# Kernel tuning notes

Hardware: AMD Instinct MI355X
Metric: run time of the kernel (lower is better)

Reference implementation:

```python
import jax, jax.numpy as jnp
import numpy as np

ROPE_BASE = 10000.0


def _rope(x):
    # x: (B, S, H, D) -- rotate-half RoPE applied per head over the sequence dim
    B, S, H, D = x.shape
    half = D // 2
    inv_freq = 1.0 / (ROPE_BASE ** (jnp.arange(half, dtype=jnp.float32) / half))
    ang = jnp.arange(S, dtype=jnp.float32)[:, None] * inv_freq[None, :]  # (S, half)
    cos = jnp.cos(ang)[None, :, None, :].astype(x.dtype)
    sin = jnp.sin(ang)[None, :, None, :].astype(x.dtype)
    x1, x2 = x[..., :half], x[..., half:]
    return jnp.concatenate([x1 * cos - x2 * sin, x2 * cos + x1 * sin], axis=-1)


def setup_inputs() -> dict:
    key = jax.random.key(0)
    ks = jax.random.split(key, 7)
    B, S, D = 8, 1024, 512
    HD = 512  # num_heads * key_dim = 8 * 64
    scale = 0.02
    return {
        "query": jax.random.normal(ks[0], (B, S, D), dtype=jnp.float32),
        "value": jax.random.normal(ks[1], (B, S, D), dtype=jnp.float32),
        "key_in": jax.random.normal(ks[2], (B, S, D), dtype=jnp.float32),
        "Wq": jax.random.normal(ks[3], (D, HD), dtype=jnp.float32) * scale,
        "Wk": jax.random.normal(ks[4], (D, HD), dtype=jnp.float32) * scale,
        "Wv": jax.random.normal(ks[5], (D, HD), dtype=jnp.float32) * scale,
        "Wo": jax.random.normal(ks[6], (HD, D), dtype=jnp.float32) * scale,
    }


def reference(query, value, key_in, Wq, Wk, Wv, Wo):
    H, Dh = 8, 64
    B, Sq, _ = query.shape
    Sk = key_in.shape[1]
    # QKV projections, split heads: (B, S, H, Dh)
    q = (query @ Wq).reshape(B, Sq, H, Dh)
    v = (value @ Wv).reshape(B, Sk, H, Dh)
    k = (key_in @ Wk).reshape(B, Sk, H, Dh)
    # inline RoPE on q and k (applied before head transpose, as in the original)
    q = _rope(q)
    k = _rope(k)
    # scaled dot-product attention with causal mask
    q = q * (1.0 / jnp.sqrt(jnp.asarray(Dh, q.dtype)))
    scores = jnp.einsum("bqhd,bkhd->bhqk", q, k)  # (B, H, Sq, Sk)
    causal = jnp.tril(jnp.ones((Sq, Sk), dtype=bool))[None, None]
    scores = jnp.where(causal, scores, jnp.asarray(-1e9, scores.dtype))
    probs = jax.nn.softmax(scores, axis=-1)
    out = jnp.einsum("bhqk,bkhd->bqhd", probs, v)  # (B, Sq, H, Dh)
    out = out.reshape(B, Sq, H * Dh) @ Wo  # output projection
    return out
```

## Files before the change

### kernel.cpp

```cpp
#include <hip/hip_runtime.h>
#include <hip/hip_bf16.h>
#include <stdint.h>

#define DEV static __device__ __forceinline__

typedef __attribute__((ext_vector_type(8)))  short    s16x8;
typedef __attribute__((ext_vector_type(4)))  short    s16x4;
typedef __attribute__((ext_vector_type(8)))  __bf16   bf16x8;
typedef __attribute__((ext_vector_type(2)))  __bf16   bf16x2;
typedef __attribute__((ext_vector_type(4)))  float    f32x4;
typedef __attribute__((ext_vector_type(16))) float    f32x16;
typedef __attribute__((ext_vector_type(2)))  unsigned u32x2;
typedef __attribute__((ext_vector_type(4)))  unsigned u32x4;

#define WAIT_VMCNT(N) do{ asm volatile("s_waitcnt vmcnt(" #N ")" ::: "memory"); \
                          __builtin_amdgcn_sched_barrier(0); }while(0)
DEV void barrier_raw(){ __builtin_amdgcn_sched_barrier(0); __builtin_amdgcn_s_barrier(); }

DEV short f2b(float f){
  union{float f; uint32_t i;} x; x.f = f;
  uint32_t r = x.i + 0x7FFFu + ((x.i >> 16) & 1u);
  return (short)(r >> 16);
}
DEV unsigned packbf(float a, float b){
  bf16x2 v = { (__bf16)a, (__bf16)b };
  return __builtin_bit_cast(unsigned, v);
}
DEV bf16x8 as_bf(s16x8 v){ return __builtin_bit_cast(bf16x8, v); }
DEV float fexp2(float x){ return __builtin_amdgcn_exp2f(x); }
DEV f32x4 mf(s16x8 a, s16x8 b, f32x4 c){
  return __builtin_amdgcn_mfma_f32_16x16x32_bf16(as_bf(a), as_bf(b), c, 0, 0, 0);
}
DEV f32x16 mf32(s16x8 a, s16x8 b, f32x16 c){
  return __builtin_amdgcn_mfma_f32_32x32x16_bf16(as_bf(a), as_bf(b), c, 0, 0, 0);
}

DEV void gload_lds16(const void* g, void* l){
  __builtin_amdgcn_global_load_lds((const __attribute__((address_space(1))) void*)g,
                                   (__attribute__((address_space(3))) void*)l, 16, 0, 0);
}

#if __has_builtin(__builtin_amdgcn_permlane32_swap)
DEV void pswap2(unsigned a, unsigned b, unsigned& x, unsigned& y){
  u32x2 rr = __builtin_amdgcn_permlane32_swap(a, b, false, false);
  x = rr[0]; y = rr[1];
}
DEV float partner32(float v, int hi){
  unsigned u = __builtin_bit_cast(unsigned, v);
  u32x2 rr = __builtin_amdgcn_permlane32_swap(u, u, false, false);
  return __builtin_bit_cast(float, hi ? rr[0] : rr[1]);
}
#else
DEV void pswap2(unsigned a, unsigned b, unsigned& x, unsigned& y){
  unsigned pa_ = (unsigned)__shfl_xor((int)a, 32, 64);
  unsigned pb_ = (unsigned)__shfl_xor((int)b, 32, 64);
  int lo = ((threadIdx.x & 63) < 32);
  x = lo ? a   : pb_;
  y = lo ? pa_ : b;
}
DEV float partner32(float v, int hi){ (void)hi; return __shfl_xor(v, 32, 64); }
#endif

__global__ __launch_bounds__(256) void k_conv3(const float* __restrict__ q,
                                               const float* __restrict__ k,
                                               const float* __restrict__ v,
                                               short* __restrict__ out){
  int z = blockIdx.z;
  const float* in = (z == 0) ? q : (z == 1) ? k : v;
  int i = (blockIdx.x * 256 + threadIdx.x) * 4;
  float4 val = *(const float4*)(in + i);
  short o[4] = { f2b(val.x), f2b(val.y), f2b(val.z), f2b(val.w) };
  *(uint2*)(out + (size_t)z * 4194304 + i) = *(uint2*)o;
}

__global__ __launch_bounds__(256) void k_wt4(const float* __restrict__ w0,
                                             const float* __restrict__ w1,
                                             const float* __restrict__ w2,
                                             const float* __restrict__ w3,
                                             short* __restrict__ wt){
  __shared__ float tile[32][33];
  int z = blockIdx.z;
  const float* w = (z == 0) ? w0 : (z == 1) ? w1 : (z == 2) ? w2 : w3;
  short* o = wt + (size_t)z * 262144;
  int bx = blockIdx.x * 32, by = blockIdx.y * 32;
  int tx = threadIdx.x, ty = threadIdx.y;
  for (int j = 0; j < 32; j += 8)
    tile[ty + j][tx] = w[(size_t)(by + ty + j) * 512 + bx + tx];
  __syncthreads();
  for (int j = 0; j < 32; j += 8)
    o[(size_t)(bx + ty + j) * 512 + by + tx] = f2b(tile[tx][ty + j]);
}

__global__ __launch_bounds__(256) void k_table(float* __restrict__ tab){
  int idx = blockIdx.x * 256 + threadIdx.x;
  int s = idx >> 5, j = idx & 31;
  float inv = __expf(-(float)j * (1.0f / 32.0f) * logf(10000.0f));
  float ang = (float)s * inv;
  tab[idx * 2 + 0] = cosf(ang);
  tab[idx * 2 + 1] = sinf(ang);
}

__global__ __launch_bounds__(256) void k_qkv(const short* __restrict__ Xb,
                                             const short* __restrict__ Wcat,
                                             const float* __restrict__ tab,
                                             short* __restrict__ Qa,
                                             short* __restrict__ Ka,
                                             short* __restrict__ Vt){
  __shared__ __align__(16) short Al[3][4096];
  __shared__ __align__(16) short Bl[3][4096];
  const int t = threadIdx.x, w = t >> 6, lane = t & 63, fr = lane & 15, fg = lane >> 4;
  const int sel = blockIdx.y >> 2;
  const short* X = Xb + (size_t)sel * 4194304;
  const int bm = blockIdx.x * 128, bn = blockIdx.y * 128;
  const int wm = (w >> 1) * 64, wn = (w & 1) * 64;

  auto stage = [&](int buf, int k0){
#pragma unroll
    for (int q = 0; q < 2; q++){
      int lin = q * 256 + t;
      int row = lin >> 2, sl = lin & 3;
      int gs = (sl ^ (row & 3)) * 8;
      gload_lds16(X    + (size_t)(bm + row) * 512 + k0 + gs, &Al[buf][(q * 256 + w * 64) * 8]);
      gload_lds16(Wcat + (size_t)(bn + row) * 512 + k0 + gs, &Bl[buf][(q * 256 + w * 64) * 8]);
    }
  };

  f32x4 acc[4][4] = {};
  stage(0, 0);
  stage(1, 32);
  for (int t16 = 0; t16 < 16; ++t16){
    barrier_raw();
    int kc = t16 + 2; if (kc > 15) kc = 15;
    stage((t16 + 2) % 3, kc * 32);
    WAIT_VMCNT(8);
    barrier_raw();
    const int cur = t16 % 3;
    s16x8 af[4], bv[4];
#pragma unroll
    for (int f = 0; f < 4; f++){
      int ra = wm + f * 16 + fr;
      af[f] = *(const s16x8*)(&Al[cur][ra * 32 + ((fg ^ (ra & 3)) * 8)]);
      int rb = wn + f * 16 + fr;
      bv[f] = *(const s16x8*)(&Bl[cur][rb * 32 + ((fg ^ (rb & 3)) * 8)]);
    }
#pragma unroll
    for (int i = 0; i < 4; i++)
#pragma unroll
      for (int jj = 0; jj < 4; jj++)
        acc[i][jj] = mf(af[i], bv[jj], acc[i][jj]);
  }

  const int row0 = bm + wm + fg * 4;
  const int b = row0 >> 10;
  const int s_base = row0 & 1023;
  const int hh = (((blockIdx.y & 3) * 128) + wn) >> 6;
  if (sel < 2){
    const float scale = (sel == 0) ? 0.125f * 1.44269504f : 1.0f;
    short* out = (sel == 0) ? Qa : Ka;
#pragma unroll
    for (int i = 0; i < 4; i++)
#pragma unroll
      for (int jj = 0; jj < 2; jj++){
        int d = jj * 16 + fr;
#pragma unroll
        for (int r = 0; r < 4; r++){
          int s = s_base + i * 16 + r;
          float2 cs = *(const float2*)(tab + (size_t)(s * 32 + d) * 2);
          float x1 = acc[i][jj][r], x2 = acc[i][jj + 2][r];
          size_t ob = ((size_t)((b * 8 + hh) * 1024 + s)) * 64 + d;
          out[ob]      = f2b((x1 * cs.x - x2 * cs.y) * scale);
          out[ob + 32] = f2b((x2 * cs.x + x1 * cs.y) * scale);
        }
      }
  } else {
#pragma unroll
    for (int i = 0; i < 4; i++)
#pragma unroll
      for (int jj = 0; jj < 4; jj++){
        int d = jj * 16 + fr;
        s16x4 pk;
#pragma unroll
        for (int r = 0; r < 4; r++) pk[r] = f2b(acc[i][jj][r]);
        size_t ob = ((size_t)((b * 8 + hh) * 64 + d)) * 1024 + s_base + i * 16;
        *(s16x4*)(Vt + ob) = pk;
      }
  }
}

__global__ __launch_bounds__(256) void k_attn(const short* __restrict__ Qb,
                                              const short* __restrict__ Kb,
                                              const short* __restrict__ Vt,
                                              short* __restrict__ O){
  __shared__ __align__(16) short KL[3][4096];
  __shared__ __align__(16) short VL[3][4096];
  const int bid = blockIdx.x;
  const int BiMap[8] = {7,6,5,4, 0,1,2,3};
  const int Bi = BiMap[bid >> 6];
  const int bh = bid & 63;
  const int B0 = Bi * 128;
  const int nch = (B0 >> 6) + 2;
  const int t = threadIdx.x, w = t >> 6, lane = t & 63;
  const int col = lane & 31, hi = lane >> 5;
  const short* Qp = Qb + (size_t)bh * 65536;
  const short* Kp = Kb + (size_t)bh * 65536;
  const short* Vp = Vt + (size_t)bh * 65536;
  const int qrow = B0 + 4 * col + w;

  s16x8 qb[4];
#pragma unroll
  for (int ks = 0; ks < 4; ks++)
    qb[ks] = *(const s16x8*)(Qp + (size_t)qrow * 64 + ks * 16 + hi * 8);

  int crow[16];
#pragma unroll
  for (int r = 0; r < 16; r++) crow[r] = (r & 3) + 8 * (r >> 2) + 4 * hi;

  f32x16 oacc[2] = {};
  float m = -1e30f, l = 0.f;

  auto stage = [&](int buf, int kv0){
#pragma unroll
    for (int R = 0; R < 2; R++){
      int lin = R * 256 + w * 64 + lane;
      int row = lin >> 3, slot = lin & 7;
      int gs = ((slot ^ (row & 7)) * 8);
      gload_lds16(Kp + (size_t)(kv0 + row) * 64 + gs, &KL[buf][(R * 256 + w * 64) * 8]);
      gload_lds16(Vp + (size_t)row * 1024 + kv0 + gs, &VL[buf][(R * 256 + w * 64) * 8]);
    }
  };

  stage(0, 0);
  stage(1, (nch > 1 ? 64 : 0));

  for (int i = 0; i < nch; ++i){
    const int kv0 = i * 64;
    barrier_raw();
    int kc = i + 2; if (kc > nch - 1) kc = nch - 1;
    stage((i + 2) % 3, kc * 64);
    WAIT_VMCNT(8);
    barrier_raw();
    const int cur = i % 3;
    __builtin_amdgcn_s_setprio(1);
    f32x16 sc[2];
#pragma unroll
    for (int f = 0; f < 2; f++){
      f32x16 s = {};
      int row = f * 32 + col, rx = row & 7;
#pragma unroll
      for (int ks = 0; ks < 4; ks++){
        s16x8 ka = *(const s16x8*)(&KL[cur][row * 64 + ((ks * 2 + hi) ^ rx) * 8]);
        s = mf32(ka, qb[ks], s);
      }
      sc[f] = s;
    }
    __builtin_amdgcn_s_setprio(0);
    if (kv0 >= B0){
#pragma unroll
      for (int f = 0; f < 2; f++)
#pragma unroll
        for (int r = 0; r < 16; r++){
          int kv = kv0 + f * 32 + crow[r];
          if (kv > qrow) sc[f][r] = -1e30f;
        }
    }
    float mx[16];
#pragma unroll
    for (int r = 0; r < 16; r++) mx[r] = fmaxf(sc[0][r], sc[1][r]);
#pragma unroll
    for (int off = 8; off >= 1; off >>= 1)
#pragma unroll
      for (int r = 0; r < off; r++) mx[r] = fmaxf(mx[r], mx[r + off]);
    float tm = fmaxf(mx[0], partner32(mx[0], hi));
    if (!__all(tm <= m + 8.f)){
      float mn = fmaxf(m, tm);
      float corr = fexp2(m - mn);
      m = mn;
      l *= corr;
      float cpv[16];
#pragma unroll
      for (int r = 0; r < 16; r++) cpv[r] = __shfl(corr, crow[r], 64);
#pragma unroll
      for (int r = 0; r < 16; r++){ oacc[0][r] *= cpv[r]; oacc[1][r] *= cpv[r]; }
    }
    float p[32];
#pragma unroll
    for (int f = 0; f < 2; f++)
#pragma unroll
      for (int i2 = 0; i2 < 16; i2++) p[f * 16 + i2] = fexp2(sc[f][i2] - m);
    unsigned wq[2][8];
#pragma unroll
    for (int f = 0; f < 2; f++)
#pragma unroll
      for (int i2 = 0; i2 < 8; i2++)
        wq[f][i2] = packbf(p[f * 16 + 2 * i2], p[f * 16 + 2 * i2 + 1]);
#pragma unroll
    for (int off = 16; off >= 1; off >>= 1)
#pragma unroll
      for (int r = 0; r < off; r++) p[r] += p[r + off];
    l += p[0] + partner32(p[0], hi);
    s16x8 pa[4];
#pragma unroll
    for (int f = 0; f < 2; f++)
#pragma unroll
      for (int half = 0; half < 2; half++){
        unsigned w0, w1, w2, w3;
        pswap2(wq[f][half * 4 + 0], wq[f][half * 4 + 2], w0, w2);
        pswap2(wq[f][half * 4 + 1], wq[f][half * 4 + 3], w1, w3);
        u32x4 uv = { w0, w1, w2, w3 };
        pa[f * 2 + half] = __builtin_bit_cast(s16x8, uv);
      }
    __builtin_amdgcn_s_setprio(1);
#pragma unroll
    for (int ks = 0; ks < 4; ks++)
#pragma unroll
      for (int df = 0; df < 2; df++){
        int row = df * 32 + col;
        s16x8 vb = *(const s16x8*)(&VL[cur][row * 64 + ((ks * 2 + hi) ^ (row & 7)) * 8]);
        oacc[df] = mf32(pa[ks], vb, oacc[df]);
      }
    __builtin_amdgcn_s_setprio(0);
  }

  const int b = bh >> 3, h = bh & 7;
  float lf[16];
#pragma unroll
  for (int r = 0; r < 16; r++) lf[r] = __shfl(l, crow[r], 64);
#pragma unroll
  for (int r = 0; r < 16; r++){
    int qq = B0 + 4 * crow[r] + w;
    float inv = 1.0f / lf[r];
    O[(size_t)(b * 1024 + qq) * 512 + h * 64 + col]      = f2b(oacc[0][r] * inv);
    O[(size_t)(b * 1024 + qq) * 512 + h * 64 + 32 + col] = f2b(oacc[1][r] * inv);
  }
}

__global__ __launch_bounds__(256) void k_gemm_out(const short* __restrict__ X,
                                                  const short* __restrict__ Wt,
                                                  float* __restrict__ C){
  __shared__ __align__(16) short Al[3][8192];
  __shared__ __align__(16) short Bl[3][8192];
  const int t = threadIdx.x;
  const int w = t >> 6, lane = t & 63, fr = lane & 15, fg = lane >> 4;
  const int bm = blockIdx.x * 128, bn = blockIdx.y * 128;
  const int wm = (w >> 1) * 64, wn = (w & 1) * 64;

  auto stage = [&](int buf, int k0){
#pragma unroll
    for (int q = 0; q < 4; q++){
      int lin = q * 256 + t;
      int row = lin >> 3, sl = lin & 7;
      int gs = (sl ^ (row & 7)) * 8;
      gload_lds16(X  + (size_t)(bm + row) * 512 + k0 + gs, &Al[buf][(q * 256 + w * 64) * 8]);
      gload_lds16(Wt + (size_t)(bn + row) * 512 + k0 + gs, &Bl[buf][(q * 256 + w * 64) * 8]);
    }
  };

  f32x4 acc[4][4] = {};
  stage(0, 0);
  stage(1, 64);
  for (int t8 = 0; t8 < 8; ++t8){
    barrier_raw();
    int kc = t8 + 2; if (kc > 7) kc = 7;
    stage((t8 + 2) % 3, kc * 64);
    WAIT_VMCNT(16);
    barrier_raw();
    const int cur = t8 % 3;
#pragma unroll
    for (int kk = 0; kk < 2; kk++){
      s16x8 af[4], bv[4];
#pragma unroll
      for (int f = 0; f < 4; f++){
        int rowa = wm + f * 16 + fr;
        af[f] = *(const s16x8*)(&Al[cur][rowa * 64 + ((kk * 4 + fg) ^ (rowa & 7)) * 8]);
        int rowb = wn + f * 16 + fr;
        bv[f] = *(const s16x8*)(&Bl[cur][rowb * 64 + ((kk * 4 + fg) ^ (rowb & 7)) * 8]);
      }
#pragma unroll
      for (int i = 0; i < 4; i++)
#pragma unroll
        for (int jj = 0; jj < 4; jj++)
          acc[i][jj] = mf(af[i], bv[jj], acc[i][jj]);
    }
  }
  const int row0 = bm + wm + fg * 4;
  const int col0 = bn + wn + fr;
#pragma unroll
  for (int i = 0; i < 4; i++)
#pragma unroll
    for (int jj = 0; jj < 4; jj++)
#pragma unroll
      for (int r = 0; r < 4; r++)
        C[(size_t)(row0 + i * 16 + r) * 512 + col0 + jj * 16] = acc[i][jj][r];
}

extern "C" void kernel_launch(void* const* d_in, const int* in_sizes, int n_in,
                              void* d_out, int out_size, void* d_ws, size_t ws_size,
                              hipStream_t stream){
  const float* query  = (const float*)d_in[0];
  const float* value  = (const float*)d_in[1];
  const float* key_in = (const float*)d_in[2];
  const float* Wq     = (const float*)d_in[3];
  const float* Wk     = (const float*)d_in[4];
  const float* Wv     = (const float*)d_in[5];
  const float* Wo     = (const float*)d_in[6];

  char* ws = (char*)d_ws;
  const size_t MB = 1ull << 20;
  short* Xb   = (short*)(ws);
  short* Wcat = (short*)(ws + 24 * MB);
  float* tab  = (float*)(ws + 26 * MB);
  short* Qa   = (short*)(ws + 26 * MB + 256 * 1024);
  short* Ka   = (short*)((char*)Qa + 8 * MB);
  short* Va   = (short*)((char*)Ka + 8 * MB);
  short* Oa   = Xb;
  short* Wot  = Wcat + 786432;

  k_conv3<<<dim3(4096, 1, 3), 256, 0, stream>>>(query, key_in, value, Xb);
  k_wt4<<<dim3(16, 16, 4), dim3(32, 8), 0, stream>>>(Wq, Wk, Wv, Wo, Wcat);
  k_table<<<128, 256, 0, stream>>>(tab);

  k_qkv<<<dim3(64, 12), 256, 0, stream>>>(Xb, Wcat, tab, Qa, Ka, Va);

  k_attn<<<512, 256, 0, stream>>>(Qa, Ka, Va, Oa);

  k_gemm_out<<<dim3(64, 4), 256, 0, stream>>>(Oa, Wot, (float*)d_out);
}
```

Before: 80.99 us.

## Pair causal query blocks per attention workgroup and use single-barrier pipelines

The attention kernel now gives each workgroup two query blocks, p and 7-p, so causal work is balanced across blocks. Both blocks share one K/V staging stream, which halves the launched workgroups and the redundant K/V loads. All three pipelined kernels (QKV GEMM, attention, output GEMM) also move the vmcnt wait before a single barrier instead of using two barriers per iteration. The trade-off is that holding two sets of accumulators and Q fragments raises register pressure (launch_bounds min blocks set to 1), and 256 workgroups may underfill the device.

After: 93.15 us. 1.15x slower.

```diff
diff --git a/kernel.cpp b/kernel.cpp
--- a/kernel.cpp
+++ b/kernel.cpp
@@ -129,11 +129,10 @@
   stage(0, 0);
   stage(1, 32);
   for (int t16 = 0; t16 < 16; ++t16){
+    WAIT_VMCNT(4);
     barrier_raw();
     int kc = t16 + 2; if (kc > 15) kc = 15;
     stage((t16 + 2) % 3, kc * 32);
-    WAIT_VMCNT(8);
-    barrier_raw();
     const int cur = t16 % 3;
     s16x8 af[4], bv[4];
 #pragma unroll
@@ -187,36 +186,40 @@
   }
 }
 
-__global__ __launch_bounds__(256) void k_attn(const short* __restrict__ Qb,
-                                              const short* __restrict__ Kb,
-                                              const short* __restrict__ Vt,
-                                              short* __restrict__ O){
+__global__ __launch_bounds__(256, 1) void k_attn(const short* __restrict__ Qb,
+                                                 const short* __restrict__ Kb,
+                                                 const short* __restrict__ Vt,
+                                                 short* __restrict__ O){
   __shared__ __align__(16) short KL[3][4096];
   __shared__ __align__(16) short VL[3][4096];
   const int bid = blockIdx.x;
-  const int BiMap[8] = {7,6,5,4, 0,1,2,3};
-  const int Bi = BiMap[bid >> 6];
   const int bh = bid & 63;
-  const int B0 = Bi * 128;
-  const int nch = (B0 >> 6) + 2;
+  const int p  = bid >> 6;
+  const int A0 = p * 128;
+  const int B0 = (7 - p) * 128;
+  const int nch  = (B0 >> 6) + 2;
+  const int nchA = (A0 >> 6) + 2;
   const int t = threadIdx.x, w = t >> 6, lane = t & 63;
   const int col = lane & 31, hi = lane >> 5;
   const short* Qp = Qb + (size_t)bh * 65536;
   const short* Kp = Kb + (size_t)bh * 65536;
   const short* Vp = Vt + (size_t)bh * 65536;
-  const int qrow = B0 + 4 * col + w;
-
-  s16x8 qb[4];
-#pragma unroll
-  for (int ks = 0; ks < 4; ks++)
-    qb[ks] = *(const s16x8*)(Qp + (size_t)qrow * 64 + ks * 16 + hi * 8);
+  const int qrowA = A0 + 4 * col + w;
+  const int qrowB = B0 + 4 * col + w;
+
+  s16x8 qbA[4], qbB[4];
+#pragma unroll
+  for (int ks = 0; ks < 4; ks++){
+    qbA[ks] = *(const s16x8*)(Qp + (size_t)qrowA * 64 + ks * 16 + hi * 8);
+    qbB[ks] = *(const s16x8*)(Qp + (size_t)qrowB * 64 + ks * 16 + hi * 8);
+  }
 
   int crow[16];
 #pragma unroll
   for (int r = 0; r < 16; r++) crow[r] = (r & 3) + 8 * (r >> 2) + 4 * hi;
 
-  f32x16 oacc[2] = {};
-  float m = -1e30f, l = 0.f;
+  f32x16 oA[2] = {}, oB[2] = {};
+  float mA = -1e30f, lA = 0.f, mB = -1e30f, lB = 0.f;
 
   auto stage = [&](int buf, int kv0){
 #pragma unroll
@@ -229,40 +232,8 @@
     }
   };
 
-  stage(0, 0);
-  stage(1, (nch > 1 ? 64 : 0));
-
-  for (int i = 0; i < nch; ++i){
-    const int kv0 = i * 64;
-    barrier_raw();
-    int kc = i + 2; if (kc > nch - 1) kc = nch - 1;
-    stage((i + 2) % 3, kc * 64);
-    WAIT_VMCNT(8);
-    barrier_raw();
-    const int cur = i % 3;
-    __builtin_amdgcn_s_setprio(1);
-    f32x16 sc[2];
-#pragma unroll
-    for (int f = 0; f < 2; f++){
-      f32x16 s = {};
-      int row = f * 32 + col, rx = row & 7;
-#pragma unroll
-      for (int ks = 0; ks < 4; ks++){
-        s16x8 ka = *(const s16x8*)(&KL[cur][row * 64 + ((ks * 2 + hi) ^ rx) * 8]);
-        s = mf32(ka, qb[ks], s);
-      }
-      sc[f] = s;
-    }
-    __builtin_amdgcn_s_setprio(0);
-    if (kv0 >= B0){
-#pragma unroll
-      for (int f = 0; f < 2; f++)
-#pragma unroll
-        for (int r = 0; r < 16; r++){
-          int kv = kv0 + f * 32 + crow[r];
-          if (kv > qrow) sc[f][r] = -1e30f;
-        }
-    }
+  auto softmax_pa = [&](f32x16 (&sc)[2], float& m, float& l, f32x16 (&oacc)[2],
+                        s16x8 (&pa)[4]){
     float mx[16];
 #pragma unroll
     for (int r = 0; r < 16; r++) mx[r] = fmaxf(sc[0][r], sc[1][r]);
@@ -282,23 +253,22 @@
 #pragma unroll
       for (int r = 0; r < 16; r++){ oacc[0][r] *= cpv[r]; oacc[1][r] *= cpv[r]; }
     }
-    float p[32];
+    float pp[32];
 #pragma unroll
     for (int f = 0; f < 2; f++)
 #pragma unroll
-      for (int i2 = 0; i2 < 16; i2++) p[f * 16 + i2] = fexp2(sc[f][i2] - m);
+      for (int i2 = 0; i2 < 16; i2++) pp[f * 16 + i2] = fexp2(sc[f][i2] - m);
     unsigned wq[2][8];
 #pragma unroll
     for (int f = 0; f < 2; f++)
 #pragma unroll
       for (int i2 = 0; i2 < 8; i2++)
-        wq[f][i2] = packbf(p[f * 16 + 2 * i2], p[f * 16 + 2 * i2 + 1]);
+        wq[f][i2] = packbf(pp[f * 16 + 2 * i2], pp[f * 16 + 2 * i2 + 1]);
 #pragma unroll
     for (int off = 16; off >= 1; off >>= 1)
 #pragma unroll
-      for (int r = 0; r < off; r++) p[r] += p[r + off];
-    l += p[0] + partner32(p[0], hi);
-    s16x8 pa[4];
+      for (int r = 0; r < off; r++) pp[r] += pp[r + off];
+    l += pp[0] + partner32(pp[0], hi);
 #pragma unroll
     for (int f = 0; f < 2; f++)
 #pragma unroll
@@ -309,6 +279,67 @@
         u32x4 uv = { w0, w1, w2, w3 };
         pa[f * 2 + half] = __builtin_bit_cast(s16x8, uv);
       }
+  };
+
+  stage(0, 0);
+  stage(1, 64);
+
+  for (int i = 0; i < nch; ++i){
+    const int kv0 = i * 64;
+    WAIT_VMCNT(4);
+    barrier_raw();
+    int kc = i + 2; if (kc > nch - 1) kc = nch - 1;
+    stage((i + 2) % 3, kc * 64);
+    const int cur = i % 3;
+    const bool Aact = (i < nchA);
+    __builtin_amdgcn_s_setprio(1);
+    f32x16 sB[2], sA[2];
+#pragma unroll
+    for (int f = 0; f < 2; f++){
+      int row = f * 32 + col, rx = row & 7;
+      f32x16 sb = {};
+#pragma unroll
+      for (int ks = 0; ks < 4; ks++){
+        s16x8 ka = *(const s16x8*)(&KL[cur][row * 64 + ((ks * 2 + hi) ^ rx) * 8]);
+        sb = mf32(ka, qbB[ks], sb);
+      }
+      sB[f] = sb;
+    }
+    if (Aact){
+#pragma unroll
+      for (int f = 0; f < 2; f++){
+        int row = f * 32 + col, rx = row & 7;
+        f32x16 sa = {};
+#pragma unroll
+        for (int ks = 0; ks < 4; ks++){
+          s16x8 ka = *(const s16x8*)(&KL[cur][row * 64 + ((ks * 2 + hi) ^ rx) * 8]);
+          sa = mf32(ka, qbA[ks], sa);
+        }
+        sA[f] = sa;
+      }
+    }
+    __builtin_amdgcn_s_setprio(0);
+    if (kv0 >= B0){
+#pragma unroll
+      for (int f = 0; f < 2; f++)
+#pragma unroll
+        for (int r = 0; r < 16; r++){
+          int kv = kv0 + f * 32 + crow[r];
+          if (kv > qrowB) sB[f][r] = -1e30f;
+        }
+    }
+    if (Aact && kv0 >= A0){
+#pragma unroll
+      for (int f = 0; f < 2; f++)
+#pragma unroll
+        for (int r = 0; r < 16; r++){
+          int kv = kv0 + f * 32 + crow[r];
+          if (kv > qrowA) sA[f][r] = -1e30f;
+        }
+    }
+    s16x8 paB[4], paA[4];
+    softmax_pa(sB, mB, lB, oB, paB);
+    if (Aact) softmax_pa(sA, mA, lA, oA, paA);
     __builtin_amdgcn_s_setprio(1);
 #pragma unroll
     for (int ks = 0; ks < 4; ks++)
@@ -316,7 +347,8 @@
       for (int df = 0; df < 2; df++){
         int row = df * 32 + col;
         s16x8 vb = *(const s16x8*)(&VL[cur][row * 64 + ((ks * 2 + hi) ^ (row & 7)) * 8]);
-        oacc[df] = mf32(pa[ks], vb, oacc[df]);
+        oB[df] = mf32(paB[ks], vb, oB[df]);
+        if (Aact) oA[df] = mf32(paA[ks], vb, oA[df]);
       }
     __builtin_amdgcn_s_setprio(0);
   }
@@ -324,13 +356,22 @@
   const int b = bh >> 3, h = bh & 7;
   float lf[16];
 #pragma unroll
-  for (int r = 0; r < 16; r++) lf[r] = __shfl(l, crow[r], 64);
+  for (int r = 0; r < 16; r++) lf[r] = __shfl(lB, crow[r], 64);
 #pragma unroll
   for (int r = 0; r < 16; r++){
     int qq = B0 + 4 * crow[r] + w;
     float inv = 1.0f / lf[r];
-    O[(size_t)(b * 1024 + qq) * 512 + h * 64 + col]      = f2b(oacc[0][r] * inv);
-    O[(size_t)(b * 1024 + qq) * 512 + h * 64 + 32 + col] = f2b(oacc[1][r] * inv);
+    O[(size_t)(b * 1024 + qq) * 512 + h * 64 + col]      = f2b(oB[0][r] * inv);
+    O[(size_t)(b * 1024 + qq) * 512 + h * 64 + 32 + col] = f2b(oB[1][r] * inv);
+  }
+#pragma unroll
+  for (int r = 0; r < 16; r++) lf[r] = __shfl(lA, crow[r], 64);
+#pragma unroll
+  for (int r = 0; r < 16; r++){
+    int qq = A0 + 4 * crow[r] + w;
+    float inv = 1.0f / lf[r];
+    O[(size_t)(b * 1024 + qq) * 512 + h * 64 + col]      = f2b(oA[0][r] * inv);
+    O[(size_t)(b * 1024 + qq) * 512 + h * 64 + 32 + col] = f2b(oA[1][r] * inv);
   }
 }
 
@@ -359,11 +400,10 @@
   stage(0, 0);
   stage(1, 64);
   for (int t8 = 0; t8 < 8; ++t8){
+    WAIT_VMCNT(8);
     barrier_raw();
     int kc = t8 + 2; if (kc > 7) kc = 7;
     stage((t8 + 2) % 3, kc * 64);
-    WAIT_VMCNT(16);
-    barrier_raw();
     const int cur = t8 % 3;
 #pragma unroll
     for (int kk = 0; kk < 2; kk++){
@@ -421,7 +461,7 @@
 
   k_qkv<<<dim3(64, 12), 256, 0, stream>>>(Xb, Wcat, tab, Qa, Ka, Va);
 
-  k_attn<<<512, 256, 0, stream>>>(Qa, Ka, Va, Oa);
+  k_attn<<<256, 256, 0, stream>>>(Qa, Ka, Va, Oa);
 
   k_gemm_out<<<dim3(64, 4), 256, 0, stream>>>(Oa, Wot, (float*)d_out);
 }
```
